# Kernel optimization log

Hardware: AMD Instinct MI355X
Metric: run time of the kernel (lower is better)

Reference implementation:

```python
import jax, jax.numpy as jnp
import numpy as np

N, T, H = 512, 43, 128
VOCAB, OUT = 32000, 8000
DK = 96
DFF = 2048
EPS = 1e-5


def _lin(x, W, b):
    # torch nn.Linear: y = x @ W.T + b, W: [out, in]
    return jnp.einsum('nth,oh->nto', x, W) + b


def _ln(x, g, b):
    m = jnp.mean(x, axis=-1, keepdims=True)
    v = jnp.mean((x - m) ** 2, axis=-1, keepdims=True)
    return (x - m) / jnp.sqrt(v + EPS) * g + b


def setup_inputs() -> dict:
    key = jax.random.key(0)
    ks = jax.random.split(key, 24)
    s = 0.02
    d = {
        'inputs': jax.random.randint(ks[0], (N, T), 0, VOCAB),
        'emb': jax.random.normal(ks[1], (VOCAB, H), jnp.float32) * s,
        'pos_emb': jax.random.normal(ks[2], (T, H), jnp.float32) * s,
        'Wk1': jax.random.normal(ks[3], (DK, H), jnp.float32) * s,
        'bk1': jnp.zeros((DK,), jnp.float32),
        'Wv1': jax.random.normal(ks[4], (DK, H), jnp.float32) * s,
        'bv1': jnp.zeros((DK,), jnp.float32),
        'Wq1': jax.random.normal(ks[5], (DK, H), jnp.float32) * s,
        'bq1': jnp.zeros((DK,), jnp.float32),
        'Wk2': jax.random.normal(ks[6], (DK, H), jnp.float32) * s,
        'bk2': jnp.zeros((DK,), jnp.float32),
        'Wv2': jax.random.normal(ks[7], (DK, H), jnp.float32) * s,
        'bv2': jnp.zeros((DK,), jnp.float32),
        'Wq2': jax.random.normal(ks[8], (DK, H), jnp.float32) * s,
        'bq2': jnp.zeros((DK,), jnp.float32),
        'Wproj': jax.random.normal(ks[9], (H, 2 * DK), jnp.float32) * s,
        'bproj': jnp.zeros((H,), jnp.float32),
        'g_mh': jnp.ones((H,), jnp.float32),
        'b_mh': jnp.zeros((H,), jnp.float32),
        'Wff1': jax.random.normal(ks[10], (DFF, H), jnp.float32) * s,
        'bff1': jnp.zeros((DFF,), jnp.float32),
        'Wff2': jax.random.normal(ks[11], (H, DFF), jnp.float32) * s,
        'bff2': jnp.zeros((H,), jnp.float32),
        'g_ff': jnp.ones((H,), jnp.float32),
        'b_ff': jnp.zeros((H,), jnp.float32),
        'Wfin': jax.random.normal(ks[12], (OUT, H), jnp.float32) * s,
        'bfin': jnp.zeros((OUT,), jnp.float32),
    }
    return d


def reference(inputs, emb, pos_emb, Wk1, bk1, Wv1, bv1, Wq1, bq1,
              Wk2, bk2, Wv2, bv2, Wq2, bq2, Wproj, bproj, g_mh, b_mh,
              Wff1, bff1, Wff2, bff2, g_ff, b_ff, Wfin, bfin):
    # embed: word + positional
    x = emb[inputs] + pos_emb[None, :, :]  # [N,T,H]

    # manual 2-head attention (separate projections per head)
    scale = 1.0 / np.sqrt(DK).astype(np.float32)

    def head(Wk, bk, Wv, bv, Wq, bq):
        k = _lin(x, Wk, bk)
        v = _lin(x, Wv, bv)
        q = _lin(x, Wq, bq)
        scores = jnp.einsum('ntd,nsd->nts', q, k) * scale  # [N,T,T]
        attn = jax.nn.softmax(scores, axis=-1)
        return jnp.einsum('nts,nsd->ntd', attn, v)

    h1 = head(Wk1, bk1, Wv1, bv1, Wq1, bq1)
    h2 = head(Wk2, bk2, Wv2, bv2, Wq2, bq2)
    mh = _lin(jnp.concatenate([h1, h2], axis=-1), Wproj, bproj)
    x = _ln(mh + x, g_mh, b_mh)

    # FFN + residual + LN
    ff = _lin(jax.nn.relu(_lin(x, Wff1, bff1)), Wff2, bff2)
    x = _ln(ff + x, g_ff, b_ff)

    # final projection to vocab
    return _lin(x, Wfin, bfin)  # [N,T,OUT]
```

## Files before the change

kernel.cpp:

```cpp
#include <hip/hip_runtime.h>
#include <hip/hip_bf16.h>

typedef unsigned short ushort;
typedef __attribute__((ext_vector_type(4))) float floatx4;
typedef __attribute__((ext_vector_type(8))) short short8;

constexpr int NB   = 512;
constexpr int T    = 43;
constexpr int H    = 128;
constexpr int NT   = NB * T;
constexpr int DK   = 96;
constexpr int DFF  = 2048;
constexpr int OUTD = 8000;

__device__ __forceinline__ ushort f2b(float f) {
    __hip_bfloat16 h = __float2bfloat16(f);
    return *reinterpret_cast<ushort*>(&h);
}

#define GLOAD16(g, l) __builtin_amdgcn_global_load_lds( \
    (const __attribute__((address_space(1))) unsigned int*)(g), \
    (__attribute__((address_space(3))) unsigned int*)(l), 16, 0, 0)

template<bool RELU, bool OUT_BF16>
__global__ __launch_bounds__(256) void gemm_bt(
    const ushort* __restrict__ A, const ushort* __restrict__ B,
    const float* __restrict__ bias, void* __restrict__ Cv,
    int M, int N, int K)
{
    __shared__ ushort As[128 * 32];
    __shared__ ushort Bs[128 * 32];
    const int tid  = threadIdx.x;
    const int lane = tid & 63;
    const int wm   = (tid >> 6) & 1;
    const int wn   = (tid >> 6) >> 1;
    const long tileM = (long)blockIdx.y * 128;
    const long tileN = (long)blockIdx.x * 128;

    floatx4 acc[4][4] = {};

    const ushort* ga0 = A + (tileM + (tid >> 2)) * (long)K + (tid & 3) * 8;
    const ushort* ga1 = A + (tileM + 64 + (tid >> 2)) * (long)K + (tid & 3) * 8;
    const ushort* gb0 = B + (tileN + (tid >> 2)) * (long)K + (tid & 3) * 8;
    const ushort* gb1 = B + (tileN + 64 + (tid >> 2)) * (long)K + (tid & 3) * 8;
    ushort* la0 = &As[tid * 8];
    ushort* la1 = &As[(tid + 256) * 8];
    ushort* lb0 = &Bs[tid * 8];
    ushort* lb1 = &Bs[(tid + 256) * 8];

    for (int k0 = 0; k0 < K; k0 += 32) {
        __syncthreads();
        GLOAD16(ga0 + k0, la0);
        GLOAD16(ga1 + k0, la1);
        GLOAD16(gb0 + k0, lb0);
        GLOAD16(gb1 + k0, lb1);
        __syncthreads();
        short8 af[4], bfr[4];
        #pragma unroll
        for (int mi = 0; mi < 4; ++mi)
            af[mi] = *(const short8*)&As[(wm * 64 + mi * 16 + (lane & 15)) * 32 + (lane >> 4) * 8];
        #pragma unroll
        for (int ni = 0; ni < 4; ++ni)
            bfr[ni] = *(const short8*)&Bs[(wn * 64 + ni * 16 + (lane & 15)) * 32 + (lane >> 4) * 8];
        #pragma unroll
        for (int mi = 0; mi < 4; ++mi)
            #pragma unroll
            for (int ni = 0; ni < 4; ++ni)
                acc[mi][ni] = __builtin_amdgcn_mfma_f32_16x16x32_bf16(
                    af[mi], bfr[ni], acc[mi][ni], 0, 0, 0);
    }

    const int r0 = wm * 64 + (lane >> 4) * 4;
    const int c0 = wn * 64 + (lane & 15);
    #pragma unroll
    for (int ni = 0; ni < 4; ++ni) {
        long col = tileN + c0 + ni * 16;
        if (col < N) {
            float bv = bias ? bias[col] : 0.0f;
            #pragma unroll
            for (int mi = 0; mi < 4; ++mi) {
                #pragma unroll
                for (int r = 0; r < 4; ++r) {
                    long row = tileM + r0 + mi * 16 + r;
                    float v = acc[mi][ni][r] + bv;
                    if (RELU) v = v > 0.0f ? v : 0.0f;
                    if (OUT_BF16) ((ushort*)Cv)[row * N + col] = f2b(v);
                    else          ((float*)Cv)[row * N + col] = v;
                }
            }
        }
    }
}

__global__ __launch_bounds__(256) void embed_kernel(
    const int* __restrict__ inputs, const float* __restrict__ emb,
    const float* __restrict__ pos, float* __restrict__ xf, ushort* __restrict__ xb)
{
    long i = (long)blockIdx.x * 256 + threadIdx.x;
    int h  = (int)(i & 127);
    int nt = (int)(i >> 7);
    int t  = nt % T;
    float v = emb[(long)inputs[nt] * H + h] + pos[t * H + h];
    xf[i] = v;
    xb[i] = f2b(v);
}

__global__ __launch_bounds__(256) void pack_qkv(
    const float* q1, const float* k1, const float* v1,
    const float* q2, const float* k2, const float* v2,
    const float* bq1, const float* bk1, const float* bv1,
    const float* bq2, const float* bk2, const float* bv2,
    ushort* __restrict__ W, float* __restrict__ bias)
{
    int i = blockIdx.x * 256 + threadIdx.x;
    int n = i >> 7, kk = i & 127;
    float val = 0.0f;
    if (n < 576) {
        const float* ws[6] = {q1, k1, v1, q2, k2, v2};
        val = ws[n / 96][(n % 96) * 128 + kk];
    }
    W[i] = f2b(val);
    if (kk == 0) {
        float bv = 0.0f;
        if (n < 576) {
            const float* bs[6] = {bq1, bk1, bv1, bq2, bk2, bv2};
            bv = bs[n / 96][n % 96];
        }
        bias[n] = bv;
    }
}

__global__ __launch_bounds__(256) void cvt_w(
    const float* __restrict__ src, ushort* __restrict__ dst,
    int rows, int cols, int rows_pad)
{
    long i = (long)blockIdx.x * 256 + threadIdx.x;
    if (i >= (long)rows_pad * cols) return;
    long r = i / cols;
    dst[i] = f2b(r < rows ? src[i] : 0.0f);
}

__global__ __launch_bounds__(256) void attn_kernel(
    const float* __restrict__ qkv, ushort* __restrict__ h12)
{
    const int head = blockIdx.x;
    const int n    = blockIdx.y;
    const int tid  = threadIdx.x;
    __shared__ float q[T][DK], k[T][DK], v[T][DK];
    __shared__ float s[T][T + 1];
    const float scale = 0.10206207261596575f;
    const long base = (long)n * T * 576 + head * 288;

    for (int i = tid; i < T * DK; i += 256) {
        int r = i / DK, c = i % DK;
        q[r][c] = qkv[base + r * 576 + c];
        k[r][c] = qkv[base + r * 576 + 96 + c];
        v[r][c] = qkv[base + r * 576 + 192 + c];
    }
    __syncthreads();
    for (int i = tid; i < T * T; i += 256) {
        int r = i / T, c = i % T;
        float d = 0.0f;
        #pragma unroll 8
        for (int x = 0; x < DK; ++x) d += q[r][x] * k[c][x];
        s[r][c] = d * scale;
    }
    __syncthreads();
    if (tid < T) {
        float mx = -1e30f;
        for (int j = 0; j < T; ++j) mx = fmaxf(mx, s[tid][j]);
        float sum = 0.0f;
        for (int j = 0; j < T; ++j) { float e = __expf(s[tid][j] - mx); s[tid][j] = e; sum += e; }
        float inv = 1.0f / sum;
        for (int j = 0; j < T; ++j) s[tid][j] *= inv;
    }
    __syncthreads();
    for (int i = tid; i < T * DK; i += 256) {
        int r = i / DK, c = i % DK;
        float d = 0.0f;
        #pragma unroll
        for (int j = 0; j < T; ++j) d += s[r][j] * v[j][c];
        h12[((long)n * T + r) * 192 + head * 96 + c] = f2b(d);
    }
}

__global__ __launch_bounds__(256) void ln_kernel(
    const float* __restrict__ a, const float* __restrict__ resid,
    const float* __restrict__ g, const float* __restrict__ b,
    ushort* __restrict__ out_bf, float* __restrict__ out_f32, int M)
{
    const int lane = threadIdx.x & 63;
    const int row  = blockIdx.x * 4 + (threadIdx.x >> 6);
    if (row >= M) return;
    const long o = (long)row * H;
    float v0 = a[o + lane] + resid[o + lane];
    float v1 = a[o + 64 + lane] + resid[o + 64 + lane];
    float s  = v0 + v1, sq = v0 * v0 + v1 * v1;
    #pragma unroll
    for (int w = 32; w; w >>= 1) { s += __shfl_xor(s, w, 64); sq += __shfl_xor(sq, w, 64); }
    float mean = s * (1.0f / H);
    float var  = sq * (1.0f / H) - mean * mean;
    float rstd = rsqrtf(var + 1e-5f);
    float o0 = (v0 - mean) * rstd * g[lane] + b[lane];
    float o1 = (v1 - mean) * rstd * g[64 + lane] + b[64 + lane];
    out_bf[o + lane] = f2b(o0);
    out_bf[o + 64 + lane] = f2b(o1);
    if (out_f32) { out_f32[o + lane] = o0; out_f32[o + 64 + lane] = o1; }
}

extern "C" void kernel_launch(void* const* d_in, const int* in_sizes, int n_in,
                              void* d_out, int out_size, void* d_ws, size_t ws_size,
                              hipStream_t stream)
{
    const int*   inputs  = (const int*)  d_in[0];
    const float* emb     = (const float*)d_in[1];
    const float* pos_emb = (const float*)d_in[2];
    const float* Wk1 = (const float*)d_in[3],  *bk1 = (const float*)d_in[4];
    const float* Wv1 = (const float*)d_in[5],  *bv1 = (const float*)d_in[6];
    const float* Wq1 = (const float*)d_in[7],  *bq1 = (const float*)d_in[8];
    const float* Wk2 = (const float*)d_in[9],  *bk2 = (const float*)d_in[10];
    const float* Wv2 = (const float*)d_in[11], *bv2 = (const float*)d_in[12];
    const float* Wq2 = (const float*)d_in[13], *bq2 = (const float*)d_in[14];
    const float* Wproj = (const float*)d_in[15], *bproj = (const float*)d_in[16];
    const float* g_mh  = (const float*)d_in[17], *b_mh  = (const float*)d_in[18];
    const float* Wff1  = (const float*)d_in[19], *bff1  = (const float*)d_in[20];
    const float* Wff2  = (const float*)d_in[21], *bff2  = (const float*)d_in[22];
    const float* g_ff  = (const float*)d_in[23], *b_ff  = (const float*)d_in[24];
    const float* Wfin  = (const float*)d_in[25], *bfin  = (const float*)d_in[26];

    char* scr = (char*)d_out;
    size_t soff = 0;
    auto salloc = [&](size_t bytes) {
        void* p = scr + soff;
        soff = (soff + bytes + 255) & ~(size_t)255;
        return p;
    };
    float*  x_f   = (float*) salloc((size_t)NT * H * 4);
    ushort* x_b   = (ushort*)salloc((size_t)NT * H * 2);
    float*  qkv   = (float*) salloc((size_t)NT * 576 * 4);
    ushort* h12   = (ushort*)salloc((size_t)NT * 192 * 2);
    float*  mh    = (float*) salloc((size_t)NT * H * 4);
    float*  xln_f = (float*) salloc((size_t)NT * H * 4);
    ushort* xln_b = (ushort*)salloc((size_t)NT * H * 2);
    ushort* ffa   = (ushort*)salloc((size_t)NT * DFF * 2);
    float*  ff2   = (float*) salloc((size_t)NT * H * 4);
    ushort* Wqkv  = (ushort*)salloc(640 * 128 * 2);
    float*  bqkv  = (float*) salloc(640 * 4);
    ushort* Wp_b  = (ushort*)salloc(128 * 192 * 2);
    ushort* W1_b  = (ushort*)salloc((size_t)DFF * 128 * 2);
    ushort* W2_b  = (ushort*)salloc((size_t)128 * DFF * 2);

    char* ws = (char*)d_ws;
    size_t woff = 0;
    auto walloc = [&](size_t bytes) {
        void* p = ws + woff;
        woff = (woff + bytes + 255) & ~(size_t)255;
        return p;
    };
    ushort* y_b  = (ushort*)walloc((size_t)NT * H * 2);
    ushort* Wf_b = (ushort*)walloc((size_t)8064 * 128 * 2);

    pack_qkv<<<(640 * 128) / 256, 256, 0, stream>>>(
        Wq1, Wk1, Wv1, Wq2, Wk2, Wv2, bq1, bk1, bv1, bq2, bk2, bv2, Wqkv, bqkv);
    cvt_w<<<(128 * 192) / 256, 256, 0, stream>>>(Wproj, Wp_b, 128, 192, 128);
    cvt_w<<<(DFF * 128) / 256, 256, 0, stream>>>(Wff1, W1_b, DFF, 128, DFF);
    cvt_w<<<(128 * DFF) / 256, 256, 0, stream>>>(Wff2, W2_b, 128, DFF, 128);
    cvt_w<<<(8064 * 128) / 256, 256, 0, stream>>>(Wfin, Wf_b, OUTD, 128, 8064);

    embed_kernel<<<(NT * H) / 256, 256, 0, stream>>>(inputs, emb, pos_emb, x_f, x_b);

    const int MT = NT / 128;

    gemm_bt<false, false><<<dim3(5, MT), 256, 0, stream>>>(x_b, Wqkv, bqkv, qkv, NT, 576, 128);

    attn_kernel<<<dim3(2, NB), 256, 0, stream>>>(qkv, h12);

    gemm_bt<false, false><<<dim3(1, MT), 256, 0, stream>>>(h12, Wp_b, bproj, mh, NT, 128, 192);

    ln_kernel<<<NT / 4, 256, 0, stream>>>(mh, x_f, g_mh, b_mh, xln_b, xln_f, NT);

    gemm_bt<true, true><<<dim3(DFF / 128, MT), 256, 0, stream>>>(xln_b, W1_b, bff1, ffa, NT, DFF, 128);

    gemm_bt<false, false><<<dim3(1, MT), 256, 0, stream>>>(ffa, W2_b, bff2, ff2, NT, 128, DFF);

    ln_kernel<<<NT / 4, 256, 0, stream>>>(ff2, xln_f, g_ff, b_ff, y_b, nullptr, NT);

    gemm_bt<false, false><<<dim3(63, MT), 256, 0, stream>>>(y_b, Wf_b, bfin, (float*)d_out, NT, OUTD, 128);
}
```

Before: 1.062 ms.

## Add K=128 GEMM with resident A tile, swizzled LDS, double-buffered generic GEMM

Adds a specialised GEMM for K=128 that loads the whole A tile into XOR-swizzled LDS once, keeps its fragments in registers, and loops over several N tiles per block with nontemporal stores. It is used for the QKV, FFN1 and final vocab projections. The generic GEMM gains double-buffered LDS staging so the next K slice loads while the current one computes, and the four weight-conversion launches are merged into one. The larger LDS footprint (64KB per block) may reduce occupancy. The grid for the vocab projection shrinks to 7 column blocks, which lowers parallelism in exchange for more reuse of A.

```diff
diff --git a/kernel.cpp b/kernel.cpp
--- a/kernel.cpp
+++ b/kernel.cpp
@@ -28,8 +28,8 @@
     const float* __restrict__ bias, void* __restrict__ Cv,
     int M, int N, int K)
 {
-    __shared__ ushort As[128 * 32];
-    __shared__ ushort Bs[128 * 32];
+    __shared__ ushort As[2][128 * 32];
+    __shared__ ushort Bs[2][128 * 32];
     const int tid  = threadIdx.x;
     const int lane = tid & 63;
     const int wm   = (tid >> 6) & 1;
@@ -43,32 +43,35 @@
     const ushort* ga1 = A + (tileM + 64 + (tid >> 2)) * (long)K + (tid & 3) * 8;
     const ushort* gb0 = B + (tileN + (tid >> 2)) * (long)K + (tid & 3) * 8;
     const ushort* gb1 = B + (tileN + 64 + (tid >> 2)) * (long)K + (tid & 3) * 8;
-    ushort* la0 = &As[tid * 8];
-    ushort* la1 = &As[(tid + 256) * 8];
-    ushort* lb0 = &Bs[tid * 8];
-    ushort* lb1 = &Bs[(tid + 256) * 8];
-
-    for (int k0 = 0; k0 < K; k0 += 32) {
+
+#define STAGE_BT(buf, k0) do { \
+        GLOAD16(ga0 + (k0), &As[buf][tid * 8]); \
+        GLOAD16(ga1 + (k0), &As[buf][(tid + 256) * 8]); \
+        GLOAD16(gb0 + (k0), &Bs[buf][tid * 8]); \
+        GLOAD16(gb1 + (k0), &Bs[buf][(tid + 256) * 8]); } while (0)
+
+    const int nsteps = K >> 5;
+    STAGE_BT(0, 0);
+    int cur = 0;
+    for (int t = 0; t < nsteps; ++t) {
         __syncthreads();
-        GLOAD16(ga0 + k0, la0);
-        GLOAD16(ga1 + k0, la1);
-        GLOAD16(gb0 + k0, lb0);
-        GLOAD16(gb1 + k0, lb1);
-        __syncthreads();
+        if (t + 1 < nsteps) STAGE_BT(cur ^ 1, (t + 1) * 32);
         short8 af[4], bfr[4];
         #pragma unroll
         for (int mi = 0; mi < 4; ++mi)
-            af[mi] = *(const short8*)&As[(wm * 64 + mi * 16 + (lane & 15)) * 32 + (lane >> 4) * 8];
+            af[mi] = *(const short8*)&As[cur][(wm * 64 + mi * 16 + (lane & 15)) * 32 + (lane >> 4) * 8];
         #pragma unroll
         for (int ni = 0; ni < 4; ++ni)
-            bfr[ni] = *(const short8*)&Bs[(wn * 64 + ni * 16 + (lane & 15)) * 32 + (lane >> 4) * 8];
+            bfr[ni] = *(const short8*)&Bs[cur][(wn * 64 + ni * 16 + (lane & 15)) * 32 + (lane >> 4) * 8];
         #pragma unroll
         for (int mi = 0; mi < 4; ++mi)
             #pragma unroll
             for (int ni = 0; ni < 4; ++ni)
                 acc[mi][ni] = __builtin_amdgcn_mfma_f32_16x16x32_bf16(
                     af[mi], bfr[ni], acc[mi][ni], 0, 0, 0);
-    }
+        cur ^= 1;
+    }
+#undef STAGE_BT
 
     const int r0 = wm * 64 + (lane >> 4) * 4;
     const int c0 = wn * 64 + (lane & 15);
@@ -92,6 +95,101 @@
     }
 }
 
+template<int NTPB, bool RELU, bool OUT_BF16, bool NTS>
+__global__ __launch_bounds__(256, 2) void gemm_k128(
+    const ushort* __restrict__ A, const ushort* __restrict__ B,
+    const float* __restrict__ bias, void* __restrict__ Cv, int N)
+{
+    __shared__ ushort As[128 * 128];
+    __shared__ ushort Bs[128 * 128];
+    const int tid  = threadIdx.x;
+    const int lane = tid & 63;
+    const int wm   = (tid >> 6) & 1;
+    const int wn   = (tid >> 7);
+    const long tileM  = (long)blockIdx.y * 128;
+    const long tileN0 = (long)blockIdx.x * (NTPB * 128);
+
+    #pragma unroll
+    for (int c = 0; c < 8; ++c) {
+        int idx = c * 256 + tid;
+        int row = idx >> 4;
+        int sw  = ((idx & 15) * 16) ^ ((row & 7) << 4);
+        const char* src = (const char*)A + (tileM + row) * 256 + sw;
+        GLOAD16(src, &As[idx * 8]);
+    }
+    __syncthreads();
+
+    short8 af[4][4];
+    const int seg16 = (lane >> 4) * 16;
+    #pragma unroll
+    for (int mi = 0; mi < 4; ++mi) {
+        int r  = wm * 64 + mi * 16 + (lane & 15);
+        int xr = (r & 7) << 4;
+        #pragma unroll
+        for (int kk = 0; kk < 4; ++kk)
+            af[mi][kk] = *(const short8*)((const char*)As + r * 256 + ((kk * 64 + seg16) ^ xr));
+    }
+
+    for (int j = 0; j < NTPB; ++j) {
+        const long tileN = tileN0 + j * 128;
+        __syncthreads();
+        #pragma unroll
+        for (int c = 0; c < 8; ++c) {
+            int idx = c * 256 + tid;
+            int row = idx >> 4;
+            int sw  = ((idx & 15) * 16) ^ ((row & 7) << 4);
+            const char* src = (const char*)B + (tileN + row) * 256 + sw;
+            GLOAD16(src, &Bs[idx * 8]);
+        }
+        __syncthreads();
+
+        floatx4 acc[4][4] = {};
+        #pragma unroll
+        for (int kk = 0; kk < 4; ++kk) {
+            short8 bfr[4];
+            #pragma unroll
+            for (int ni = 0; ni < 4; ++ni) {
+                int r  = wn * 64 + ni * 16 + (lane & 15);
+                int xr = (r & 7) << 4;
+                bfr[ni] = *(const short8*)((const char*)Bs + r * 256 + ((kk * 64 + seg16) ^ xr));
+            }
+            #pragma unroll
+            for (int mi = 0; mi < 4; ++mi)
+                #pragma unroll
+                for (int ni = 0; ni < 4; ++ni)
+                    acc[mi][ni] = __builtin_amdgcn_mfma_f32_16x16x32_bf16(
+                        af[mi][kk], bfr[ni], acc[mi][ni], 0, 0, 0);
+        }
+
+        const int r0 = wm * 64 + (lane >> 4) * 4;
+        const int c0 = wn * 64 + (lane & 15);
+        #pragma unroll
+        for (int ni = 0; ni < 4; ++ni) {
+            long col = tileN + c0 + ni * 16;
+            if (col < N) {
+                float bv = bias ? bias[col] : 0.0f;
+                #pragma unroll
+                for (int mi = 0; mi < 4; ++mi) {
+                    #pragma unroll
+                    for (int r = 0; r < 4; ++r) {
+                        long row = tileM + r0 + mi * 16 + r;
+                        float v = acc[mi][ni][r] + bv;
+                        if (RELU) v = v > 0.0f ? v : 0.0f;
+                        if (OUT_BF16) {
+                            ushort hv = f2b(v);
+                            ushort* p = (ushort*)Cv + row * N + col;
+                            if (NTS) __builtin_nontemporal_store(hv, p); else *p = hv;
+                        } else {
+                            float* p = (float*)Cv + row * N + col;
+                            if (NTS) __builtin_nontemporal_store(v, p); else *p = v;
+                        }
+                    }
+                }
+            }
+        }
+    }
+}
+
 __global__ __launch_bounds__(256) void embed_kernel(
     const int* __restrict__ inputs, const float* __restrict__ emb,
     const float* __restrict__ pos, float* __restrict__ xf, ushort* __restrict__ xb)
@@ -130,14 +228,27 @@
     }
 }
 
-__global__ __launch_bounds__(256) void cvt_w(
-    const float* __restrict__ src, ushort* __restrict__ dst,
-    int rows, int cols, int rows_pad)
-{
-    long i = (long)blockIdx.x * 256 + threadIdx.x;
-    if (i >= (long)rows_pad * cols) return;
-    long r = i / cols;
-    dst[i] = f2b(r < rows ? src[i] : 0.0f);
+__global__ __launch_bounds__(256) void cvt_all(
+    const float* __restrict__ Wproj, const float* __restrict__ Wff1,
+    const float* __restrict__ Wff2,  const float* __restrict__ Wfin,
+    ushort* __restrict__ Wp_b, ushort* __restrict__ W1_b,
+    ushort* __restrict__ W2_b, ushort* __restrict__ Wf_b)
+{
+    const int b = blockIdx.x, tid = threadIdx.x;
+    if (b < 96) {
+        int i = b * 256 + tid;
+        Wp_b[i] = f2b(Wproj[i]);
+    } else if (b < 1120) {
+        int i = (b - 96) * 256 + tid;
+        W1_b[i] = f2b(Wff1[i]);
+    } else if (b < 2144) {
+        int i = (b - 1120) * 256 + tid;
+        W2_b[i] = f2b(Wff2[i]);
+    } else {
+        long i = (long)(b - 2144) * 256 + tid;
+        long r = i >> 7;
+        Wf_b[i] = f2b(r < OUTD ? Wfin[i] : 0.0f);
+    }
 }
 
 __global__ __launch_bounds__(256) void attn_kernel(
@@ -262,16 +373,14 @@
 
     pack_qkv<<<(640 * 128) / 256, 256, 0, stream>>>(
         Wq1, Wk1, Wv1, Wq2, Wk2, Wv2, bq1, bk1, bv1, bq2, bk2, bv2, Wqkv, bqkv);
-    cvt_w<<<(128 * 192) / 256, 256, 0, stream>>>(Wproj, Wp_b, 128, 192, 128);
-    cvt_w<<<(DFF * 128) / 256, 256, 0, stream>>>(Wff1, W1_b, DFF, 128, DFF);
-    cvt_w<<<(128 * DFF) / 256, 256, 0, stream>>>(Wff2, W2_b, 128, DFF, 128);
-    cvt_w<<<(8064 * 128) / 256, 256, 0, stream>>>(Wfin, Wf_b, OUTD, 128, 8064);
+    cvt_all<<<6176, 256, 0, stream>>>(Wproj, Wff1, Wff2, Wfin, Wp_b, W1_b, W2_b, Wf_b);
 
     embed_kernel<<<(NT * H) / 256, 256, 0, stream>>>(inputs, emb, pos_emb, x_f, x_b);
 
     const int MT = NT / 128;
 
-    gemm_bt<false, false><<<dim3(5, MT), 256, 0, stream>>>(x_b, Wqkv, bqkv, qkv, NT, 576, 128);
+    gemm_k128<1, false, false, true><<<dim3(5, MT), 256, 0, stream>>>(
+        x_b, Wqkv, bqkv, qkv, 576);
 
     attn_kernel<<<dim3(2, NB), 256, 0, stream>>>(qkv, h12);
 
@@ -279,11 +388,13 @@
 
     ln_kernel<<<NT / 4, 256, 0, stream>>>(mh, x_f, g_mh, b_mh, xln_b, xln_f, NT);
 
-    gemm_bt<true, true><<<dim3(DFF / 128, MT), 256, 0, stream>>>(xln_b, W1_b, bff1, ffa, NT, DFF, 128);
+    gemm_k128<4, true, true, true><<<dim3(4, MT), 256, 0, stream>>>(
+        xln_b, W1_b, bff1, ffa, DFF);
 
     gemm_bt<false, false><<<dim3(1, MT), 256, 0, stream>>>(ffa, W2_b, bff2, ff2, NT, 128, DFF);
 
     ln_kernel<<<NT / 4, 256, 0, stream>>>(ff2, xln_f, g_ff, b_ff, y_b, nullptr, NT);
 
-    gemm_bt<false, false><<<dim3(63, MT), 256, 0, stream>>>(y_b, Wf_b, bfin, (float*)d_out, NT, OUTD, 128);
-}
+    gemm_k128<9, false, false, true><<<dim3(7, MT), 256, 0, stream>>>(
+        y_b, Wf_b, bfin, (float*)d_out, OUTD);
+}
```

New measurement: 1.154 ms. 1.09x slower.

## Fuse residual LayerNorm into GEMM epilogues, merge prep kernels, nontemporal final stores

Applied to the files above, without the earlier changes.

The two H=128-output GEMMs (proj, FF2) now compute bias, residual add and LayerNorm in their epilogue. Row statistics are reduced with shuffles plus a small LDS exchange across the two column-warps, which removes the separate ln kernels and the fp32 mh/ff2 round trips. All weight conversion and embedding kernels are merged into a single prep launch to cut launch overhead. The final vocab GEMM writes its large fp32 output with nontemporal stores to reduce cache pollution. The trade-off is higher register pressure from holding all tile values for the epilogue LN.

```diff
diff --git a/kernel.cpp b/kernel.cpp
--- a/kernel.cpp
+++ b/kernel.cpp
@@ -22,7 +22,7 @@
     (const __attribute__((address_space(1))) unsigned int*)(g), \
     (__attribute__((address_space(3))) unsigned int*)(l), 16, 0, 0)
 
-template<bool RELU, bool OUT_BF16>
+template<bool RELU, bool OUT_BF16, bool NTS>
 __global__ __launch_bounds__(256) void gemm_bt(
     const ushort* __restrict__ A, const ushort* __restrict__ B,
     const float* __restrict__ bias, void* __restrict__ Cv,
@@ -43,17 +43,13 @@
     const ushort* ga1 = A + (tileM + 64 + (tid >> 2)) * (long)K + (tid & 3) * 8;
     const ushort* gb0 = B + (tileN + (tid >> 2)) * (long)K + (tid & 3) * 8;
     const ushort* gb1 = B + (tileN + 64 + (tid >> 2)) * (long)K + (tid & 3) * 8;
-    ushort* la0 = &As[tid * 8];
-    ushort* la1 = &As[(tid + 256) * 8];
-    ushort* lb0 = &Bs[tid * 8];
-    ushort* lb1 = &Bs[(tid + 256) * 8];
 
     for (int k0 = 0; k0 < K; k0 += 32) {
         __syncthreads();
-        GLOAD16(ga0 + k0, la0);
-        GLOAD16(ga1 + k0, la1);
-        GLOAD16(gb0 + k0, lb0);
-        GLOAD16(gb1 + k0, lb1);
+        GLOAD16(ga0 + k0, &As[tid * 8]);
+        GLOAD16(ga1 + k0, &As[(tid + 256) * 8]);
+        GLOAD16(gb0 + k0, &Bs[tid * 8]);
+        GLOAD16(gb1 + k0, &Bs[(tid + 256) * 8]);
         __syncthreads();
         short8 af[4], bfr[4];
         #pragma unroll
@@ -84,60 +80,191 @@
                     long row = tileM + r0 + mi * 16 + r;
                     float v = acc[mi][ni][r] + bv;
                     if (RELU) v = v > 0.0f ? v : 0.0f;
-                    if (OUT_BF16) ((ushort*)Cv)[row * N + col] = f2b(v);
-                    else          ((float*)Cv)[row * N + col] = v;
+                    if (OUT_BF16) {
+                        ushort hv = f2b(v);
+                        ushort* p = (ushort*)Cv + row * N + col;
+                        if (NTS) __builtin_nontemporal_store(hv, p); else *p = hv;
+                    } else {
+                        float* p = (float*)Cv + row * N + col;
+                        if (NTS) __builtin_nontemporal_store(v, p); else *p = v;
+                    }
                 }
             }
         }
     }
 }
 
-__global__ __launch_bounds__(256) void embed_kernel(
+template<bool WRITE_F32>
+__global__ __launch_bounds__(256) void gemm_ln(
+    const ushort* __restrict__ A, const ushort* __restrict__ B,
+    const float* __restrict__ bias, const float* __restrict__ resid,
+    const float* __restrict__ g, const float* __restrict__ bvec,
+    ushort* __restrict__ out_bf, float* __restrict__ out_f32, int K)
+{
+    __shared__ ushort As[128 * 32];
+    __shared__ ushort Bs[128 * 32];
+    const int tid  = threadIdx.x;
+    const int lane = tid & 63;
+    const int wm   = (tid >> 6) & 1;
+    const int wn   = (tid >> 6) >> 1;
+    const long tileM = (long)blockIdx.x * 128;
+
+    floatx4 acc[4][4] = {};
+
+    const ushort* ga0 = A + (tileM + (tid >> 2)) * (long)K + (tid & 3) * 8;
+    const ushort* ga1 = A + (tileM + 64 + (tid >> 2)) * (long)K + (tid & 3) * 8;
+    const ushort* gb0 = B + ((tid >> 2)) * (long)K + (tid & 3) * 8;
+    const ushort* gb1 = B + (64 + (tid >> 2)) * (long)K + (tid & 3) * 8;
+
+    for (int k0 = 0; k0 < K; k0 += 32) {
+        __syncthreads();
+        GLOAD16(ga0 + k0, &As[tid * 8]);
+        GLOAD16(ga1 + k0, &As[(tid + 256) * 8]);
+        GLOAD16(gb0 + k0, &Bs[tid * 8]);
+        GLOAD16(gb1 + k0, &Bs[(tid + 256) * 8]);
+        __syncthreads();
+        short8 af[4], bfr[4];
+        #pragma unroll
+        for (int mi = 0; mi < 4; ++mi)
+            af[mi] = *(const short8*)&As[(wm * 64 + mi * 16 + (lane & 15)) * 32 + (lane >> 4) * 8];
+        #pragma unroll
+        for (int ni = 0; ni < 4; ++ni)
+            bfr[ni] = *(const short8*)&Bs[(wn * 64 + ni * 16 + (lane & 15)) * 32 + (lane >> 4) * 8];
+        #pragma unroll
+        for (int mi = 0; mi < 4; ++mi)
+            #pragma unroll
+            for (int ni = 0; ni < 4; ++ni)
+                acc[mi][ni] = __builtin_amdgcn_mfma_f32_16x16x32_bf16(
+                    af[mi], bfr[ni], acc[mi][ni], 0, 0, 0);
+    }
+
+    const int r0 = wm * 64 + (lane >> 4) * 4;
+    const int c0 = wn * 64 + (lane & 15);
+    float vals[4][4][4];
+    float rs[4][4] = {};
+    float rq[4][4] = {};
+    #pragma unroll
+    for (int ni = 0; ni < 4; ++ni) {
+        int col = c0 + ni * 16;
+        float bv = bias[col];
+        #pragma unroll
+        for (int mi = 0; mi < 4; ++mi)
+            #pragma unroll
+            for (int r = 0; r < 4; ++r) {
+                long row = tileM + r0 + mi * 16 + r;
+                float v = (acc[mi][ni][r] + bv) + resid[row * H + col];
+                vals[mi][ni][r] = v;
+                rs[mi][r] += v;
+                rq[mi][r] += v * v;
+            }
+    }
+    #pragma unroll
+    for (int mi = 0; mi < 4; ++mi)
+        #pragma unroll
+        for (int r = 0; r < 4; ++r) {
+            float s = rs[mi][r], q = rq[mi][r];
+            #pragma unroll
+            for (int m = 1; m < 16; m <<= 1) {
+                s += __shfl_xor(s, m, 64);
+                q += __shfl_xor(q, m, 64);
+            }
+            rs[mi][r] = s; rq[mi][r] = q;
+        }
+    float* sp = (float*)As;
+    float* sq = (float*)As + 256;
+    __syncthreads();
+    if ((lane & 15) == 0) {
+        #pragma unroll
+        for (int mi = 0; mi < 4; ++mi)
+            #pragma unroll
+            for (int r = 0; r < 4; ++r) {
+                int row = r0 + mi * 16 + r;
+                sp[wn * 128 + row] = rs[mi][r];
+                sq[wn * 128 + row] = rq[mi][r];
+            }
+    }
+    __syncthreads();
+    #pragma unroll
+    for (int mi = 0; mi < 4; ++mi)
+        #pragma unroll
+        for (int r = 0; r < 4; ++r) {
+            int row = r0 + mi * 16 + r;
+            float s = sp[row] + sp[128 + row];
+            float q = sq[row] + sq[128 + row];
+            float mean = s * (1.0f / H);
+            float var  = q * (1.0f / H) - mean * mean;
+            rs[mi][r] = mean;
+            rq[mi][r] = rsqrtf(var + 1e-5f);
+        }
+    #pragma unroll
+    for (int ni = 0; ni < 4; ++ni) {
+        int col = c0 + ni * 16;
+        float gv = g[col], bb = bvec[col];
+        #pragma unroll
+        for (int mi = 0; mi < 4; ++mi)
+            #pragma unroll
+            for (int r = 0; r < 4; ++r) {
+                long row = tileM + r0 + mi * 16 + r;
+                float o = (vals[mi][ni][r] - rs[mi][r]) * rq[mi][r] * gv + bb;
+                out_bf[row * H + col] = f2b(o);
+                if (WRITE_F32) out_f32[row * H + col] = o;
+            }
+    }
+}
+
+__global__ __launch_bounds__(256) void prep_kernel(
     const int* __restrict__ inputs, const float* __restrict__ emb,
-    const float* __restrict__ pos, float* __restrict__ xf, ushort* __restrict__ xb)
-{
-    long i = (long)blockIdx.x * 256 + threadIdx.x;
-    int h  = (int)(i & 127);
-    int nt = (int)(i >> 7);
-    int t  = nt % T;
-    float v = emb[(long)inputs[nt] * H + h] + pos[t * H + h];
-    xf[i] = v;
-    xb[i] = f2b(v);
-}
-
-__global__ __launch_bounds__(256) void pack_qkv(
+    const float* __restrict__ pos, float* __restrict__ xf, ushort* __restrict__ xb,
     const float* q1, const float* k1, const float* v1,
     const float* q2, const float* k2, const float* v2,
     const float* bq1, const float* bk1, const float* bv1,
     const float* bq2, const float* bk2, const float* bv2,
-    ushort* __restrict__ W, float* __restrict__ bias)
-{
-    int i = blockIdx.x * 256 + threadIdx.x;
-    int n = i >> 7, kk = i & 127;
-    float val = 0.0f;
-    if (n < 576) {
-        const float* ws[6] = {q1, k1, v1, q2, k2, v2};
-        val = ws[n / 96][(n % 96) * 128 + kk];
-    }
-    W[i] = f2b(val);
-    if (kk == 0) {
-        float bv = 0.0f;
+    ushort* __restrict__ Wqkv, float* __restrict__ bqkv,
+    const float* __restrict__ Wproj, const float* __restrict__ Wff1,
+    const float* __restrict__ Wff2,  const float* __restrict__ Wfin,
+    ushort* __restrict__ Wp_b, ushort* __restrict__ W1_b,
+    ushort* __restrict__ W2_b, ushort* __restrict__ Wf_b)
+{
+    const int b = blockIdx.x, tid = threadIdx.x;
+    if (b < 11008) {
+        long i = (long)b * 256 + tid;
+        int h  = (int)(i & 127);
+        int nt = (int)(i >> 7);
+        int t  = nt % T;
+        float v = emb[(long)inputs[nt] * H + h] + pos[t * H + h];
+        xf[i] = v;
+        xb[i] = f2b(v);
+    } else if (b < 11328) {
+        int i = (b - 11008) * 256 + tid;
+        int n = i >> 7, kk = i & 127;
+        float val = 0.0f;
         if (n < 576) {
-            const float* bs[6] = {bq1, bk1, bv1, bq2, bk2, bv2};
-            bv = bs[n / 96][n % 96];
-        }
-        bias[n] = bv;
-    }
-}
-
-__global__ __launch_bounds__(256) void cvt_w(
-    const float* __restrict__ src, ushort* __restrict__ dst,
-    int rows, int cols, int rows_pad)
-{
-    long i = (long)blockIdx.x * 256 + threadIdx.x;
-    if (i >= (long)rows_pad * cols) return;
-    long r = i / cols;
-    dst[i] = f2b(r < rows ? src[i] : 0.0f);
+            const float* ws[6] = {q1, k1, v1, q2, k2, v2};
+            val = ws[n / 96][(n % 96) * 128 + kk];
+        }
+        Wqkv[i] = f2b(val);
+        if (kk == 0) {
+            float bv = 0.0f;
+            if (n < 576) {
+                const float* bs[6] = {bq1, bk1, bv1, bq2, bk2, bv2};
+                bv = bs[n / 96][n % 96];
+            }
+            bqkv[n] = bv;
+        }
+    } else if (b < 11424) {
+        int i = (b - 11328) * 256 + tid;
+        Wp_b[i] = f2b(Wproj[i]);
+    } else if (b < 12448) {
+        int i = (b - 11424) * 256 + tid;
+        W1_b[i] = f2b(Wff1[i]);
+    } else if (b < 13472) {
+        int i = (b - 12448) * 256 + tid;
+        W2_b[i] = f2b(Wff2[i]);
+    } else {
+        long i = (long)(b - 13472) * 256 + tid;
+        long r = i >> 7;
+        Wf_b[i] = f2b(r < OUTD ? Wfin[i] : 0.0f);
+    }
 }
 
 __global__ __launch_bounds__(256) void attn_kernel(
@@ -182,30 +309,6 @@
         for (int j = 0; j < T; ++j) d += s[r][j] * v[j][c];
         h12[((long)n * T + r) * 192 + head * 96 + c] = f2b(d);
     }
-}
-
-__global__ __launch_bounds__(256) void ln_kernel(
-    const float* __restrict__ a, const float* __restrict__ resid,
-    const float* __restrict__ g, const float* __restrict__ b,
-    ushort* __restrict__ out_bf, float* __restrict__ out_f32, int M)
-{
-    const int lane = threadIdx.x & 63;
-    const int row  = blockIdx.x * 4 + (threadIdx.x >> 6);
-    if (row >= M) return;
-    const long o = (long)row * H;
-    float v0 = a[o + lane] + resid[o + lane];
-    float v1 = a[o + 64 + lane] + resid[o + 64 + lane];
-    float s  = v0 + v1, sq = v0 * v0 + v1 * v1;
-    #pragma unroll
-    for (int w = 32; w; w >>= 1) { s += __shfl_xor(s, w, 64); sq += __shfl_xor(sq, w, 64); }
-    float mean = s * (1.0f / H);
-    float var  = sq * (1.0f / H) - mean * mean;
-    float rstd = rsqrtf(var + 1e-5f);
-    float o0 = (v0 - mean) * rstd * g[lane] + b[lane];
-    float o1 = (v1 - mean) * rstd * g[64 + lane] + b[64 + lane];
-    out_bf[o + lane] = f2b(o0);
-    out_bf[o + 64 + lane] = f2b(o1);
-    if (out_f32) { out_f32[o + lane] = o0; out_f32[o + 64 + lane] = o1; }
 }
 
 extern "C" void kernel_launch(void* const* d_in, const int* in_sizes, int n_in,
@@ -239,11 +342,9 @@
     ushort* x_b   = (ushort*)salloc((size_t)NT * H * 2);
     float*  qkv   = (float*) salloc((size_t)NT * 576 * 4);
     ushort* h12   = (ushort*)salloc((size_t)NT * 192 * 2);
-    float*  mh    = (float*) salloc((size_t)NT * H * 4);
     float*  xln_f = (float*) salloc((size_t)NT * H * 4);
     ushort* xln_b = (ushort*)salloc((size_t)NT * H * 2);
     ushort* ffa   = (ushort*)salloc((size_t)NT * DFF * 2);
-    float*  ff2   = (float*) salloc((size_t)NT * H * 4);
     ushort* Wqkv  = (ushort*)salloc(640 * 128 * 2);
     float*  bqkv  = (float*) salloc(640 * 4);
     ushort* Wp_b  = (ushort*)salloc(128 * 192 * 2);
@@ -260,30 +361,27 @@
     ushort* y_b  = (ushort*)walloc((size_t)NT * H * 2);
     ushort* Wf_b = (ushort*)walloc((size_t)8064 * 128 * 2);
 
-    pack_qkv<<<(640 * 128) / 256, 256, 0, stream>>>(
-        Wq1, Wk1, Wv1, Wq2, Wk2, Wv2, bq1, bk1, bv1, bq2, bk2, bv2, Wqkv, bqkv);
-    cvt_w<<<(128 * 192) / 256, 256, 0, stream>>>(Wproj, Wp_b, 128, 192, 128);
-    cvt_w<<<(DFF * 128) / 256, 256, 0, stream>>>(Wff1, W1_b, DFF, 128, DFF);
-    cvt_w<<<(128 * DFF) / 256, 256, 0, stream>>>(Wff2, W2_b, 128, DFF, 128);
-    cvt_w<<<(8064 * 128) / 256, 256, 0, stream>>>(Wfin, Wf_b, OUTD, 128, 8064);
-
-    embed_kernel<<<(NT * H) / 256, 256, 0, stream>>>(inputs, emb, pos_emb, x_f, x_b);
-
     const int MT = NT / 128;
 
-    gemm_bt<false, false><<<dim3(5, MT), 256, 0, stream>>>(x_b, Wqkv, bqkv, qkv, NT, 576, 128);
+    prep_kernel<<<17504, 256, 0, stream>>>(
+        inputs, emb, pos_emb, x_f, x_b,
+        Wq1, Wk1, Wv1, Wq2, Wk2, Wv2, bq1, bk1, bv1, bq2, bk2, bv2,
+        Wqkv, bqkv, Wproj, Wff1, Wff2, Wfin, Wp_b, W1_b, W2_b, Wf_b);
+
+    gemm_bt<false, false, false><<<dim3(5, MT), 256, 0, stream>>>(
+        x_b, Wqkv, bqkv, qkv, NT, 576, 128);
 
     attn_kernel<<<dim3(2, NB), 256, 0, stream>>>(qkv, h12);
 
-    gemm_bt<false, false><<<dim3(1, MT), 256, 0, stream>>>(h12, Wp_b, bproj, mh, NT, 128, 192);
-
-    ln_kernel<<<NT / 4, 256, 0, stream>>>(mh, x_f, g_mh, b_mh, xln_b, xln_f, NT);
-
-    gemm_bt<true, true><<<dim3(DFF / 128, MT), 256, 0, stream>>>(xln_b, W1_b, bff1, ffa, NT, DFF, 128);
-
-    gemm_bt<false, false><<<dim3(1, MT), 256, 0, stream>>>(ffa, W2_b, bff2, ff2, NT, 128, DFF);
-
-    ln_kernel<<<NT / 4, 256, 0, stream>>>(ff2, xln_f, g_ff, b_ff, y_b, nullptr, NT);
-
-    gemm_bt<false, false><<<dim3(63, MT), 256, 0, stream>>>(y_b, Wf_b, bfin, (float*)d_out, NT, OUTD, 128);
-}
+    gemm_ln<true><<<MT, 256, 0, stream>>>(
+        h12, Wp_b, bproj, x_f, g_mh, b_mh, xln_b, xln_f, 192);
+
+    gemm_bt<true, true, false><<<dim3(16, MT), 256, 0, stream>>>(
+        xln_b, W1_b, bff1, ffa, NT, DFF, 128);
+
+    gemm_ln<false><<<MT, 256, 0, stream>>>(
+        ffa, W2_b, bff2, xln_f, g_ff, b_ff, y_b, nullptr, DFF);
+
+    gemm_bt<false, false, true><<<dim3(63, MT), 256, 0, stream>>>(
+        y_b, Wf_b, bfin, (float*)d_out, NT, OUTD, 128);
+}
```

Result: faster. 1.033 ms (-2.7%).
